# Performance work log

Hardware: AMD Instinct MI355X
Metric: run time of the kernel (lower is better)

Reference implementation:

```python
import jax, jax.numpy as jnp
import numpy as np

GRID_DIMS = (64, 64, 64)
GRID_LOWER = np.array([0.0, 0.0, 0.0], np.float32)
GRID_STEPS = np.array([0.015625, 0.015625, 0.015625], np.float32)
RADIUS = 0.03125
STENCIL = 2  # ceil(radius / step)


def _poly6(d2, h):
    # standard SPH poly6 smoothing kernel: 315/(64 pi h^9) (h^2 - d^2)^3, d <= h
    c = np.float32(315.0 / (64.0 * np.pi * h ** 9))
    return jnp.where(d2 <= h * h, c * (h * h - d2) ** 3, 0.0)


def particles2grid(locs, data, density):
    # locs [B,N,3], data [B,N,C], density [B,N] -> grid [B,X,Y,Z,C]
    B, N, _ = locs.shape
    C = data.shape[-1]
    X, Y, Z = GRID_DIMS
    dims = jnp.array(GRID_DIMS, jnp.int32)
    r = jnp.arange(-STENCIL, STENCIL + 1)
    offs = jnp.stack(jnp.meshgrid(r, r, r, indexing='ij'), -1).reshape(-1, 3)  # [K,3]
    base = jnp.floor((locs - GRID_LOWER) / GRID_STEPS).astype(jnp.int32)        # [B,N,3]
    cells = base[:, :, None, :] + offs                                          # [B,N,K,3]
    centers = GRID_LOWER + (cells.astype(locs.dtype) + 0.5) * GRID_STEPS
    d2 = jnp.sum((centers - locs[:, :, None, :]) ** 2, -1)                      # [B,N,K]
    w = _poly6(d2, RADIUS)
    w = jnp.where(jnp.all((cells >= 0) & (cells < dims), -1), w, 0.0)
    contrib = w[..., None] * (data / density[..., None])[:, :, None, :]         # [B,N,K,C]
    cells = jnp.clip(cells, 0, dims - 1)
    flat = (cells[..., 0] * Y + cells[..., 1]) * Z + cells[..., 2]              # [B,N,K]

    def splat(f, c):
        return jnp.zeros((X * Y * Z, C), data.dtype).at[f.reshape(-1)].add(c.reshape(-1, C))

    return jax.vmap(splat)(flat, contrib).reshape(B, X, Y, Z, C)


def grid2particles(grid, locs):
    # trilinear interpolation of grid [B,X,Y,Z,C] at particle locations [B,N,3]
    B, X, Y, Z, C = grid.shape
    dims = jnp.array([X, Y, Z], jnp.int32)
    pos = (locs - GRID_LOWER) / GRID_STEPS - 0.5                                # cell-center coords
    i0 = jnp.floor(pos).astype(jnp.int32)
    frac = pos - i0.astype(locs.dtype)
    gflat = grid.reshape(B, X * Y * Z, C)
    gather = jax.vmap(lambda g, f: g[f])                                        # [B,N] -> [B,N,C]
    out = jnp.zeros((B, locs.shape[1], C), grid.dtype)
    for dx in (0, 1):
        for dy in (0, 1):
            for dz in (0, 1):
                off = jnp.array([dx, dy, dz], jnp.int32)
                idx = i0 + off
                wd = jnp.where(off == 1, frac, 1.0 - frac)                      # [B,N,3]
                w = wd[..., 0] * wd[..., 1] * wd[..., 2]
                w = jnp.where(jnp.all((idx >= 0) & (idx < dims), -1), w, 0.0)
                idx = jnp.clip(idx, 0, dims - 1)
                flat = (idx[..., 0] * Y + idx[..., 1]) * Z + idx[..., 2]
                out = out + w[..., None] * gather(gflat, flat)
    return out


def conv3d(x, w, b):
    y = jax.lax.conv_general_dilated(x, w, (1, 1, 1), 'SAME',
                                     dimension_numbers=('NCDHW', 'OIDHW', 'NCDHW'))
    return y + b[None, :, None, None, None]


def prelu(x, a):
    return jnp.where(x >= 0, x, a * x)


def setup_inputs() -> dict:
    key = jax.random.key(0)
    ks = jax.random.split(key, 8)
    B, N = 2, 32768
    Cin, K, Cout = 4, 32, 4
    s = lambda fan: np.float32(1.0 / np.sqrt(fan * 27))
    return {
        'locs': jax.random.uniform(ks[0], (B, N, 3), jnp.float32),
        'data': jax.random.normal(ks[1], (B, N, Cin), jnp.float32),
        'density': jax.random.uniform(ks[2], (B, N), jnp.float32, 0.5, 1.5),
        'W0': jax.random.normal(ks[3], (K, Cin, 3, 3, 3), jnp.float32) * s(Cin),
        'b0': jnp.zeros((K,), jnp.float32),
        'W1': jax.random.normal(ks[4], (K, K, 3, 3, 3), jnp.float32) * s(K),
        'b1': jnp.zeros((K,), jnp.float32),
        'W2': jax.random.normal(ks[5], (K, K, 3, 3, 3), jnp.float32) * s(K),
        'b2': jnp.zeros((K,), jnp.float32),
        'W3': jax.random.normal(ks[6], (Cout, K, 3, 3, 3), jnp.float32) * s(K),
        'b3': jnp.zeros((Cout,), jnp.float32),
        'a0': jnp.full((1,), 0.25, jnp.float32),
        'a1': jnp.full((1,), 0.25, jnp.float32),
        'a2': jnp.full((1,), 0.25, jnp.float32),
    }


def reference(locs, data, density, W0, b0, W1, b1, W2, b2, W3, b3, a0, a1, a2):
    grid = particles2grid(locs, data, density)            # [B,X,Y,Z,Cin]
    g = jnp.transpose(grid, (0, 4, 1, 2, 3))              # NCDHW
    g = prelu(conv3d(g, W0, b0), a0)
    g = prelu(conv3d(g, W1, b1), a1)
    g = prelu(conv3d(g, W2, b2), a2)
    g = conv3d(g, W3, b3)
    g = jnp.transpose(g, (0, 2, 3, 4, 1))                 # [B,X,Y,Z,Cout]
    return grid2particles(g, locs)                        # [B,N,Cout]
```

## Files before the change

kernel.cpp:

```cpp
#include <hip/hip_runtime.h>

#define BATCH 2
#define NPART 32768
#define GD 64
#define NVOX (BATCH * GD * GD * GD)

typedef unsigned short ushortT;
typedef __attribute__((ext_vector_type(8))) short short8;
typedef __attribute__((ext_vector_type(16))) float float16;

__device__ __forceinline__ float poly6_c() {
    const double H9 = 1.0 / 35184372088832.0;
    return (float)(315.0 / (64.0 * 3.14159265358979323846 * H9));
}

__device__ __forceinline__ ushortT bf16_rne(float f) {
    unsigned int u = __float_as_uint(f);
    u = (u + 0x7fffu + ((u >> 16) & 1u)) >> 16;
    return (ushortT)u;
}

__device__ __forceinline__ int imax(int a, int b) { return a > b ? a : b; }
__device__ __forceinline__ int imin(int a, int b) { return a < b ? a : b; }

__device__ __forceinline__ void load_lds16(const void* g, void* l) {
    __builtin_amdgcn_global_load_lds(
        (const __attribute__((address_space(1))) void*)g,
        (__attribute__((address_space(3))) void*)l, 16, 0, 0);
}

__global__ void zero_ints_kernel(int* __restrict__ p, int n) {
    int t = blockIdx.x * blockDim.x + threadIdx.x;
    if (t < n) p[t] = 0;
}

__global__ __launch_bounds__(256) void bin_count_kernel(
    const float* __restrict__ locs, int* __restrict__ counts) {
    int t = blockIdx.x * blockDim.x + threadIdx.x;
    if (t >= BATCH * NPART) return;
    int b = t >> 15;
    int bx = ((int)floorf(locs[t * 3 + 0] * 64.0f)) >> 1;
    int by = ((int)floorf(locs[t * 3 + 1] * 64.0f)) >> 1;
    int bz = ((int)floorf(locs[t * 3 + 2] * 64.0f)) >> 1;
    atomicAdd(&counts[b * 32768 + ((bx * 32) + by) * 32 + bz], 1);
}

__global__ __launch_bounds__(256) void scanA_kernel(
    const int* __restrict__ counts, int* __restrict__ offsets,
    int* __restrict__ blockSum) {
    __shared__ int sh[256];
    int tid = threadIdx.x, g = blockIdx.x;
    int v = counts[g * 256 + tid];
    sh[tid] = v;
    __syncthreads();
    for (int off = 1; off < 256; off <<= 1) {
        int u = (tid >= off) ? sh[tid - off] : 0;
        __syncthreads();
        sh[tid] += u;
        __syncthreads();
    }
    offsets[g * 256 + tid] = sh[tid] - v;
    if (tid == 255) blockSum[g] = sh[255];
}

__global__ __launch_bounds__(256) void scanB_kernel(
    int* __restrict__ offsets, const int* __restrict__ blockSum) {
    __shared__ int sh[256];
    int tid = threadIdx.x, g = blockIdx.x;
    sh[tid] = (tid < g) ? blockSum[tid] : 0;
    __syncthreads();
    for (int off = 128; off > 0; off >>= 1) {
        if (tid < off) sh[tid] += sh[tid + off];
        __syncthreads();
    }
    offsets[g * 256 + tid] += sh[0];
    if (g == 255 && tid == 255) offsets[65536] = BATCH * NPART;
}

__global__ __launch_bounds__(256) void bin_scatter_kernel(
    const float* __restrict__ locs, const float* __restrict__ data,
    const float* __restrict__ density, const int* __restrict__ offsets,
    int* __restrict__ cursor, float* __restrict__ payload) {
    int t = blockIdx.x * blockDim.x + threadIdx.x;
    if (t >= BATCH * NPART) return;
    int b = t >> 15;
    float px = locs[t * 3 + 0];
    float py = locs[t * 3 + 1];
    float pz = locs[t * 3 + 2];
    int bx = ((int)floorf(px * 64.0f)) >> 1;
    int by = ((int)floorf(py * 64.0f)) >> 1;
    int bz = ((int)floorf(pz * 64.0f)) >> 1;
    int bb = b * 32768 + ((bx * 32) + by) * 32 + bz;
    int slot = atomicAdd(&cursor[bb], 1);
    int idx = offsets[bb] + slot;
    float inv_d = 1.0f / density[t];
    float4 p0 = {px, py, pz, data[t * 4 + 0] * inv_d};
    float4 p1 = {data[t * 4 + 1] * inv_d, data[t * 4 + 2] * inv_d,
                 data[t * 4 + 3] * inv_d, 0.f};
    *(float4*)(payload + idx * 8)     = p0;
    *(float4*)(payload + idx * 8 + 4) = p1;
}

__global__ __launch_bounds__(256) void splat_gather_kernel(
    const float* __restrict__ payload, const int* __restrict__ offsets,
    ushortT* __restrict__ g8) {
    __shared__ float plist[256 * 8];
    __shared__ int segS[36];
    __shared__ int segP[37];
    __shared__ int shTot[1];

    int wg = blockIdx.x;
    int sb = wg & 511, b = wg >> 9;
    int X0 = (sb >> 6) * 8, Y0 = ((sb >> 3) & 7) * 8, Z0 = (sb & 7) * 8;
    int tid = threadIdx.x;

    int bxlo = imax(0, (X0 - 2) >> 1), bxhi = imin(31, (X0 + 9) >> 1);
    int bylo = imax(0, (Y0 - 2) >> 1), byhi = imin(31, (Y0 + 9) >> 1);
    int bzlo = imax(0, (Z0 - 2) >> 1), bzhi = imin(31, (Z0 + 9) >> 1);
    int ny = byhi - bylo + 1;
    int ns = (bxhi - bxlo + 1) * ny;
    if (tid < ns) {
        int bx = bxlo + tid / ny, by = bylo + tid % ny;
        int row = b * 32768 + (bx * 32 + by) * 32;
        int s = offsets[row + bzlo];
        int e = offsets[row + bzhi + 1];
        segS[tid] = s;
        segP[tid] = e - s;
    }
    __syncthreads();
    if (tid == 0) {
        int p = 0;
        for (int k = 0; k < ns; ++k) { int len = segP[k]; segP[k] = p; p += len; }
        segP[ns] = p;
        shTot[0] = p;
    }
    __syncthreads();

    const float step = 0.015625f;
    const float h2 = 0.03125f * 0.03125f;
    const float cc = poly6_c();
    int total = shTot[0];

    int l = tid & 63, w = tid >> 6;
    int cx = X0 + 4 * (w >> 1) + (l >> 4);
    int cy = Y0 + 4 * (w & 1) + ((l >> 2) & 3);
    int cz0 = Z0 + (l & 3);
    float xc  = ((float)cx  + 0.5f) * step;
    float yc  = ((float)cy  + 0.5f) * step;
    float zc0 = ((float)cz0 + 0.5f) * step;
    float zc1 = zc0 + 4.0f * step;

    float a00 = 0.f, a01 = 0.f, a02 = 0.f, a03 = 0.f;
    float a10 = 0.f, a11 = 0.f, a12 = 0.f, a13 = 0.f;

    int nchunks = (total + 255) >> 8;
    for (int ch = 0; ch < nchunks; ++ch) {
        __syncthreads();
        int jj = (ch << 8) + tid;
        if (jj < total) {
            int k = 0;
            while (jj >= segP[k + 1]) ++k;
            int idx = segS[k] + (jj - segP[k]);
            *(float4*)(plist + tid * 8)     = *(const float4*)(payload + idx * 8);
            *(float4*)(plist + tid * 8 + 4) = *(const float4*)(payload + idx * 8 + 4);
        }
        __syncthreads();
        int cnt = imin(256, total - (ch << 8));
        for (int p = 0; p < cnt; ++p) {
            float4 pa = *(const float4*)(plist + p * 8);
            float dx = pa.x - xc, dy = pa.y - yc;
            float dxy2 = fmaf(dy, dy, dx * dx);
            if (!__any(dxy2 <= h2)) continue;
            float4 pv = *(const float4*)(plist + p * 8 + 4);
            float dz0 = pa.z - zc0;
            float d20 = fmaf(dz0, dz0, dxy2);
            float u0 = fmaxf(h2 - d20, 0.f);
            float w0 = (cc * u0) * (u0 * u0);
            a00 = fmaf(w0, pa.w, a00);
            a01 = fmaf(w0, pv.x, a01);
            a02 = fmaf(w0, pv.y, a02);
            a03 = fmaf(w0, pv.z, a03);
            float dz1 = pa.z - zc1;
            float d21 = fmaf(dz1, dz1, dxy2);
            float u1 = fmaxf(h2 - d21, 0.f);
            float w1 = (cc * u1) * (u1 * u1);
            a10 = fmaf(w1, pa.w, a10);
            a11 = fmaf(w1, pv.x, a11);
            a12 = fmaf(w1, pv.y, a12);
            a13 = fmaf(w1, pv.z, a13);
        }
    }

    size_t cellBase = (size_t)(((b * 64 + cx) * 64 + cy) * 64);
    short8 o;
    o[0] = (short)bf16_rne(a00); o[1] = (short)bf16_rne(a01);
    o[2] = (short)bf16_rne(a02); o[3] = (short)bf16_rne(a03);
    o[4] = 0; o[5] = 0; o[6] = 0; o[7] = 0;
    *(short8*)(g8 + (cellBase + cz0) * 8) = o;
    o[0] = (short)bf16_rne(a10); o[1] = (short)bf16_rne(a11);
    o[2] = (short)bf16_rne(a12); o[3] = (short)bf16_rne(a13);
    *(short8*)(g8 + (cellBase + cz0 + 4) * 8) = o;
}

__global__ void repack_all_kernel(
    const float* __restrict__ W0, const float* __restrict__ W1,
    const float* __restrict__ W2, const float* __restrict__ W3,
    short* __restrict__ Bp) {
    int t = blockIdx.x * blockDim.x + threadIdx.x;
    if (t >= 176 * 512) return;
    int kt = t >> 9;
    const float* W; int O, I, CINP, ktL;
    if (kt < 14)       { W = W0; O = 32; I = 4;  CINP = 8;  ktL = kt; }
    else if (kt < 68)  { W = W1; O = 32; I = 32; CINP = 32; ktL = kt - 14; }
    else if (kt < 122) { W = W2; O = 32; I = 32; CINP = 32; ktL = kt - 68; }
    else               { W = W3; O = 4;  I = 32; CINP = 32; ktL = kt - 122; }
    int l = (t >> 3) & 63, j = t & 7;
    int n = l & 31, q = l >> 5;
    int k = ktL * 16 + 8 * q + j;
    int tap = k / CINP;
    int ic  = k - tap * CINP;
    float v = 0.f;
    if (tap < 27 && ic < I && n < O) v = W[(n * I + ic) * 27 + tap];
    Bp[t] = (short)bf16_rne(v);
}

template <int ICG, int KT, bool FINAL>
__global__ __launch_bounds__(256) void mfma_conv_kernel(
    const ushortT* __restrict__ in, const short* __restrict__ Bpack,
    const float* __restrict__ bias, const float* __restrict__ alpha,
    const float* __restrict__ zguard, void* __restrict__ outv) {
    constexpr int CIN = ICG * 8;
    constexpr int NCH = 16 * ICG * 34;
    __shared__ short lds[NCH * 8];
    int wg = ((blockIdx.x & 7) << 9) | (blockIdx.x >> 3);
    int zh = wg & 1, yp = (wg >> 1) & 31, xp = (wg >> 6) & 31, b = wg >> 11;
    int X0 = xp * 2, Y0 = yp * 2, Z0 = zh * 32;
    int tid = threadIdx.x;

    const ushortT* inb = in + (size_t)b * (64 * 64 * 64 * CIN);
#pragma unroll
    for (int it = 0; it < (NCH + 255) / 256; ++it) {
        int ccid = it * 256 + tid;
        if (ccid < NCH) {
            int col = ccid / (ICG * 34);
            int rem = ccid - col * (ICG * 34);
            int icg = rem / 34;
            int zi  = rem - icg * 34;
            int gx = X0 + (col >> 2) - 1;
            int gy = Y0 + (col & 3) - 1;
            int gz = Z0 + zi - 1;
            const void* src = (const void*)zguard;
            if ((unsigned)gx < 64u && (unsigned)gy < 64u && (unsigned)gz < 64u)
                src = (const void*)(inb + ((size_t)(((gx * 64) + gy) * 64 + gz)) * CIN + icg * 8);
            load_lds16(src, (void*)(lds + ccid * 8));
        }
    }
    __syncthreads();

    int l = tid & 63, w = tid >> 6;
    int wx = w >> 1, wy = w & 1;
    int n = l & 31, q = l >> 5;

    float bval = FINAL ? (n < 4 ? bias[n] : 0.f) : bias[n];
    float16 acc;
#pragma unroll
    for (int r = 0; r < 16; ++r) acc[r] = bval;

    const short* bp = Bpack + (size_t)l * 8;
    int laneZ = (l & 31) * 8;

#pragma unroll
    for (int kt = 0; kt < KT; ++kt) {
        short8 bfrag = *(const short8*)(bp + kt * 512);
        int aofs;
        if constexpr (ICG == 1) {
            int tap0 = kt * 2, tap1 = kt * 2 + 1;
            if (tap1 > 26) tap1 = 26;
            int dx0 = tap0 / 9, r0 = tap0 - dx0 * 9, dy0 = r0 / 3, dz0 = r0 - dy0 * 3;
            int dx1 = tap1 / 9, r1 = tap1 - dx1 * 9, dy1 = r1 / 3, dz1 = r1 - dy1 * 3;
            int c0 = (((wx + dx0) * 4 + (wy + dy0)) * 34 + dz0) * 8;
            int c1 = (((wx + dx1) * 4 + (wy + dy1)) * 34 + dz1) * 8;
            aofs = q ? c1 : c0;
        } else {
            int tap = kt >> 1;
            int dx = tap / 9, rr = tap - dx * 9, dy = rr / 3, dz = rr - dy * 3;
            int icg = (kt & 1) * 2 + q;
            aofs = ((((wx + dx) * 4 + (wy + dy)) * ICG + icg) * 34 + dz) * 8;
        }
        short8 afrag = *(const short8*)(lds + aofs + laneZ);
        acc = __builtin_amdgcn_mfma_f32_32x32x16_bf16(afrag, bfrag, acc, 0, 0, 0);
    }

    size_t base = (size_t)(((b * 64 + X0 + wx) * 64 + (Y0 + wy)) * 64) + Z0;
    if (FINAL) {
        float* out = (float*)outv;
        if (n < 4) {
#pragma unroll
            for (int r = 0; r < 16; ++r) {
                int z = (r & 3) + 8 * (r >> 2) + 4 * q;
                out[(base + z) * 4 + n] = acc[r];
            }
        }
    } else {
        float a = alpha[0];
        ushortT* out = (ushortT*)outv;
#pragma unroll
        for (int r = 0; r < 16; ++r) {
            int z = (r & 3) + 8 * (r >> 2) + 4 * q;
            float v = acc[r];
            v = v >= 0.f ? v : a * v;
            out[(base + z) * 32 + n] = bf16_rne(v);
        }
    }
}

__global__ __launch_bounds__(256) void gather_kernel(
    const float* __restrict__ grid, const float* __restrict__ locs,
    float* __restrict__ out) {
    int t = blockIdx.x * blockDim.x + threadIdx.x;
    if (t >= BATCH * NPART) return;
    int b = t >> 15;

    float px = locs[t * 3 + 0] * 64.0f - 0.5f;
    float py = locs[t * 3 + 1] * 64.0f - 0.5f;
    float pz = locs[t * 3 + 2] * 64.0f - 0.5f;
    int ix = (int)floorf(px);
    int iy = (int)floorf(py);
    int iz = (int)floorf(pz);
    float fx = px - (float)ix;
    float fy = py - (float)iy;
    float fz = pz - (float)iz;

    const float* gb = grid + (size_t)b * GD * GD * GD * 4;
    float o0 = 0.f, o1 = 0.f, o2 = 0.f, o3 = 0.f;

#pragma unroll
    for (int dx = 0; dx < 2; ++dx) {
        int x = ix + dx;
        if ((unsigned)x > 63u) continue;
        float wx = dx ? fx : 1.0f - fx;
#pragma unroll
        for (int dy = 0; dy < 2; ++dy) {
            int y = iy + dy;
            if ((unsigned)y > 63u) continue;
            float wy = dy ? fy : 1.0f - fy;
#pragma unroll
            for (int dz = 0; dz < 2; ++dz) {
                int z = iz + dz;
                if ((unsigned)z > 63u) continue;
                float wz = dz ? fz : 1.0f - fz;
                float w = wx * wy * wz;
                const float4 g = *(const float4*)(gb + (size_t)(((x * GD) + y) * GD + z) * 4);
                o0 += w * g.x; o1 += w * g.y; o2 += w * g.z; o3 += w * g.w;
            }
        }
    }
    out[t * 4 + 0] = o0;
    out[t * 4 + 1] = o1;
    out[t * 4 + 2] = o2;
    out[t * 4 + 3] = o3;
}

extern "C" void kernel_launch(void* const* d_in, const int* in_sizes, int n_in,
                              void* d_out, int out_size, void* d_ws, size_t ws_size,
                              hipStream_t stream) {
    const float* locs    = (const float*)d_in[0];
    const float* data    = (const float*)d_in[1];
    const float* density = (const float*)d_in[2];
    const float* W0 = (const float*)d_in[3];
    const float* b0 = (const float*)d_in[4];
    const float* W1 = (const float*)d_in[5];
    const float* b1 = (const float*)d_in[6];
    const float* W2 = (const float*)d_in[7];
    const float* b2 = (const float*)d_in[8];
    const float* W3 = (const float*)d_in[9];
    const float* b3 = (const float*)d_in[10];
    const float* a0 = (const float*)d_in[11];
    const float* a1 = (const float*)d_in[12];
    const float* a2 = (const float*)d_in[13];
    float* out = (float*)d_out;

    char* ws = (char*)d_ws;
    ushortT* g8  = (ushortT*)(ws);
    ushortT* gA  = (ushortT*)(ws + 8388608);
    ushortT* gB  = (ushortT*)(ws + 41943040);
    float*  gF   = (float*)(ws + 75497472);
    short*  Bp   = (short*)(ws + 83886080);
    short*  Bp0  = Bp;
    short*  Bp1  = Bp + 14 * 512;
    short*  Bp2  = Bp + 68 * 512;
    short*  Bp3  = Bp + 122 * 512;
    float* zguard   = (float*)(ws + 84066240);
    int*   counts   = (int*)(ws + 84066304);
    int*   cursor   = (int*)(ws + 84328448);
    int*   offsets  = (int*)(ws + 84590592);
    int*   blockSum = (int*)(ws + 84852752);
    float* payload  = (float*)(ws + 84853888);

    zero_ints_kernel<<<(131088 + 255) / 256, 256, 0, stream>>>((int*)zguard, 131088);
    bin_count_kernel<<<(BATCH * NPART) / 256, 256, 0, stream>>>(locs, counts);
    scanA_kernel<<<256, 256, 0, stream>>>(counts, offsets, blockSum);
    scanB_kernel<<<256, 256, 0, stream>>>(offsets, blockSum);
    bin_scatter_kernel<<<(BATCH * NPART) / 256, 256, 0, stream>>>(
        locs, data, density, offsets, cursor, payload);

    repack_all_kernel<<<(176 * 512 + 255) / 256, 256, 0, stream>>>(W0, W1, W2, W3, Bp);

    splat_gather_kernel<<<BATCH * 512, 256, 0, stream>>>(payload, offsets, g8);

    const int CGRID = 4096;
    mfma_conv_kernel< 1, 14, false><<<CGRID, 256, 0, stream>>>(g8, Bp0, b0, a0, zguard, gA);
    mfma_conv_kernel< 4, 54, false><<<CGRID, 256, 0, stream>>>(gA, Bp1, b1, a1, zguard, gB);
    mfma_conv_kernel< 4, 54, false><<<CGRID, 256, 0, stream>>>(gB, Bp2, b2, a2, zguard, gA);
    mfma_conv_kernel< 4, 54, true ><<<CGRID, 256, 0, stream>>>(gA, Bp3, b3, b3, zguard, gF);

    gather_kernel<<<(BATCH * NPART) / 256, 256, 0, stream>>>(gF, locs, out);
}
```

Before: 267.1 us.

## Enlarge conv tile to 2x4 columns, two accumulators per wave, prefetch B fragments

Each workgroup of the MFMA conv kernels now covers a 2x4 column tile instead of 2x2, and each wave computes two y-columns with two accumulators that share one B fragment load. The LDS halo tile grows from 4x4 to 4x6 columns, so the halo overhead per output drops, and the grid is halved. B fragments are prefetched four k-steps ahead through a small register ring, and launch bounds ask for 3 waves per SIMD. The cost is more LDS (about 52KB for the ICG=4 kernels), more registers, and fewer workgroups, which can reduce occupancy.

```diff
diff --git a/kernel.cpp b/kernel.cpp
--- a/kernel.cpp
+++ b/kernel.cpp
@@ -225,16 +225,16 @@
 }
 
 template <int ICG, int KT, bool FINAL>
-__global__ __launch_bounds__(256) void mfma_conv_kernel(
+__global__ __launch_bounds__(256, 3) void mfma_conv_kernel(
     const ushortT* __restrict__ in, const short* __restrict__ Bpack,
     const float* __restrict__ bias, const float* __restrict__ alpha,
     const float* __restrict__ zguard, void* __restrict__ outv) {
     constexpr int CIN = ICG * 8;
-    constexpr int NCH = 16 * ICG * 34;
+    constexpr int NCH = 24 * ICG * 34;
     __shared__ short lds[NCH * 8];
-    int wg = ((blockIdx.x & 7) << 9) | (blockIdx.x >> 3);
-    int zh = wg & 1, yp = (wg >> 1) & 31, xp = (wg >> 6) & 31, b = wg >> 11;
-    int X0 = xp * 2, Y0 = yp * 2, Z0 = zh * 32;
+    int wg = ((blockIdx.x & 7) << 8) | (blockIdx.x >> 3);
+    int zh = wg & 1, yq = (wg >> 1) & 15, xp = (wg >> 5) & 31, b = wg >> 10;
+    int X0 = xp * 2, Y0 = yq * 4, Z0 = zh * 32;
     int tid = threadIdx.x;
 
     const ushortT* inb = in + (size_t)b * (64 * 64 * 64 * CIN);
@@ -246,8 +246,8 @@
             int rem = ccid - col * (ICG * 34);
             int icg = rem / 34;
             int zi  = rem - icg * 34;
-            int gx = X0 + (col >> 2) - 1;
-            int gy = Y0 + (col & 3) - 1;
+            int gx = X0 + col / 6 - 1;
+            int gy = Y0 + col % 6 - 1;
             int gz = Z0 + zi - 1;
             const void* src = (const void*)zguard;
             if ((unsigned)gx < 64u && (unsigned)gy < 64u && (unsigned)gz < 64u)
@@ -258,47 +258,61 @@
     __syncthreads();
 
     int l = tid & 63, w = tid >> 6;
-    int wx = w >> 1, wy = w & 1;
+    int wx = w >> 1;
+    int cyA = (w & 1) * 2, cyB = cyA + 1;
     int n = l & 31, q = l >> 5;
 
     float bval = FINAL ? (n < 4 ? bias[n] : 0.f) : bias[n];
-    float16 acc;
-#pragma unroll
-    for (int r = 0; r < 16; ++r) acc[r] = bval;
+    float16 accA, accB;
+#pragma unroll
+    for (int r = 0; r < 16; ++r) { accA[r] = bval; accB[r] = bval; }
 
     const short* bp = Bpack + (size_t)l * 8;
     int laneZ = (l & 31) * 8;
 
+    short8 bf[4];
+#pragma unroll
+    for (int i = 0; i < 4; ++i) bf[i] = *(const short8*)(bp + i * 512);
+
 #pragma unroll
     for (int kt = 0; kt < KT; ++kt) {
-        short8 bfrag = *(const short8*)(bp + kt * 512);
-        int aofs;
+        short8 bcur = bf[kt & 3];
+        if (kt + 4 < KT) bf[kt & 3] = *(const short8*)(bp + (kt + 4) * 512);
+        int aofsA, aofsB;
         if constexpr (ICG == 1) {
             int tap0 = kt * 2, tap1 = kt * 2 + 1;
             if (tap1 > 26) tap1 = 26;
             int dx0 = tap0 / 9, r0 = tap0 - dx0 * 9, dy0 = r0 / 3, dz0 = r0 - dy0 * 3;
             int dx1 = tap1 / 9, r1 = tap1 - dx1 * 9, dy1 = r1 / 3, dz1 = r1 - dy1 * 3;
-            int c0 = (((wx + dx0) * 4 + (wy + dy0)) * 34 + dz0) * 8;
-            int c1 = (((wx + dx1) * 4 + (wy + dy1)) * 34 + dz1) * 8;
-            aofs = q ? c1 : c0;
+            int cA0 = (((wx + dx0) * 6 + (cyA + dy0)) * 34 + dz0) * 8;
+            int cA1 = (((wx + dx1) * 6 + (cyA + dy1)) * 34 + dz1) * 8;
+            int cB0 = (((wx + dx0) * 6 + (cyB + dy0)) * 34 + dz0) * 8;
+            int cB1 = (((wx + dx1) * 6 + (cyB + dy1)) * 34 + dz1) * 8;
+            aofsA = q ? cA1 : cA0;
+            aofsB = q ? cB1 : cB0;
         } else {
             int tap = kt >> 1;
             int dx = tap / 9, rr = tap - dx * 9, dy = rr / 3, dz = rr - dy * 3;
             int icg = (kt & 1) * 2 + q;
-            aofs = ((((wx + dx) * 4 + (wy + dy)) * ICG + icg) * 34 + dz) * 8;
-        }
-        short8 afrag = *(const short8*)(lds + aofs + laneZ);
-        acc = __builtin_amdgcn_mfma_f32_32x32x16_bf16(afrag, bfrag, acc, 0, 0, 0);
-    }
-
-    size_t base = (size_t)(((b * 64 + X0 + wx) * 64 + (Y0 + wy)) * 64) + Z0;
+            aofsA = ((((wx + dx) * 6 + (cyA + dy)) * ICG + icg) * 34 + dz) * 8;
+            aofsB = ((((wx + dx) * 6 + (cyB + dy)) * ICG + icg) * 34 + dz) * 8;
+        }
+        short8 afragA = *(const short8*)(lds + aofsA + laneZ);
+        short8 afragB = *(const short8*)(lds + aofsB + laneZ);
+        accA = __builtin_amdgcn_mfma_f32_32x32x16_bf16(afragA, bcur, accA, 0, 0, 0);
+        accB = __builtin_amdgcn_mfma_f32_32x32x16_bf16(afragB, bcur, accB, 0, 0, 0);
+    }
+
+    size_t baseA = (size_t)(((b * 64 + X0 + wx) * 64 + (Y0 + cyA)) * 64) + Z0;
+    size_t baseB = (size_t)(((b * 64 + X0 + wx) * 64 + (Y0 + cyB)) * 64) + Z0;
     if (FINAL) {
         float* out = (float*)outv;
         if (n < 4) {
 #pragma unroll
             for (int r = 0; r < 16; ++r) {
                 int z = (r & 3) + 8 * (r >> 2) + 4 * q;
-                out[(base + z) * 4 + n] = acc[r];
+                out[(baseA + z) * 4 + n] = accA[r];
+                out[(baseB + z) * 4 + n] = accB[r];
             }
         }
     } else {
@@ -307,9 +321,12 @@
 #pragma unroll
         for (int r = 0; r < 16; ++r) {
             int z = (r & 3) + 8 * (r >> 2) + 4 * q;
-            float v = acc[r];
-            v = v >= 0.f ? v : a * v;
-            out[(base + z) * 32 + n] = bf16_rne(v);
+            float vA = accA[r];
+            vA = vA >= 0.f ? vA : a * vA;
+            out[(baseA + z) * 32 + n] = bf16_rne(vA);
+            float vB = accB[r];
+            vB = vB >= 0.f ? vB : a * vB;
+            out[(baseB + z) * 32 + n] = bf16_rne(vB);
         }
     }
 }
@@ -408,7 +425,7 @@
 
     splat_gather_kernel<<<BATCH * 512, 256, 0, stream>>>(payload, offsets, g8);
 
-    const int CGRID = 4096;
+    const int CGRID = 2048;
     mfma_conv_kernel< 1, 14, false><<<CGRID, 256, 0, stream>>>(g8, Bp0, b0, a0, zguard, gA);
     mfma_conv_kernel< 4, 54, false><<<CGRID, 256, 0, stream>>>(gA, Bp1, b1, a1, zguard, gB);
     mfma_conv_kernel< 4, 54, false><<<CGRID, 256, 0, stream>>>(gB, Bp2, b2, a2, zguard, gA);
```

After: 252.6 us. 5.4% less time.
